# Kernel tuning notes

Hardware: AMD Instinct MI355X
Metric: run time of the kernel (lower is better)

## Reference

```python
import jax, jax.numpy as jnp
import numpy as np

FEATURE_DIM = 68
ONE_HOT_MAX = 29  # one-hot coordinate features only for coords < 29


def _compute_encodings(height, width):
    # height, width are static Python ints
    xs = jnp.arange(width, dtype=jnp.float32)
    ys = jnp.arange(height, dtype=jnp.float32)

    def axis_feats(coords, size):
        if size > 1:
            norm = 2.0 * (coords / (size - 1)) - 1.0
            angle = jnp.pi * (coords / (size - 1))
        else:
            norm = jnp.zeros_like(coords)
            angle = jnp.zeros_like(coords)
        sign = jnp.sign(coords - size / 2.0)  # -1 / 0 / +1 around midpoint
        rtan = jnp.round(jnp.tan(angle))
        return jnp.stack([norm, sign, jnp.sin(angle), jnp.cos(angle), rtan], axis=-1)  # [size, 5]

    xf = axis_feats(xs, width)    # [W, 5] -> feature slots 0,2,4,6,8
    yf = axis_feats(ys, height)   # [H, 5] -> feature slots 1,3,5,7,9

    xb = jnp.broadcast_to(xf[None, :, :], (height, width, 5))
    yb = jnp.broadcast_to(yf[:, None, :], (height, width, 5))
    # interleave x/y features -> order x0,y0,x1,y1,... matches slots 0..9
    first10 = jnp.stack([xb, yb], axis=-1).reshape(height, width, 10)

    idx = jnp.arange(ONE_HOT_MAX)
    ohx = (xs[:, None] == idx[None, :]).astype(jnp.float32)  # [W, 29], zero rows for x >= 29
    ohy = (ys[:, None] == idx[None, :]).astype(jnp.float32)  # [H, 29]
    ohx_b = jnp.broadcast_to(ohx[None, :, :], (height, width, ONE_HOT_MAX))
    ohy_b = jnp.broadcast_to(ohy[:, None, :], (height, width, ONE_HOT_MAX))

    return jnp.concatenate([first10, ohx_b, ohy_b], axis=-1)  # [H, W, 68]


def setup_inputs() -> dict:
    key = jax.random.key(0)
    H, W, B = 512, 512, 8
    x = jax.random.normal(key, (B, H * W), dtype=jnp.float32)
    return {"x": x, "height": H, "width": W}


def reference(x, height, width):
    batch_size, seq_len = x.shape
    enc = _compute_encodings(height, width).reshape(-1, FEATURE_DIM)  # [H*W, 68]
    enc_b = jnp.broadcast_to(enc[None, :, :], (batch_size, seq_len, FEATURE_DIM))
    return jnp.concatenate([x[..., None], enc_b], axis=-1)  # [B, H*W, 69]
```

## Files before the change

kernel.cpp:

```cpp
#include <hip/hip_runtime.h>
#include <math.h>

typedef float f32x4 __attribute__((ext_vector_type(4)));

#define NF 69u
#define TILE_ROWS 64u
#define BLOCK 256u

__global__ void pe_table_kernel(const int* __restrict__ hptr,
                                const int* __restrict__ wptr,
                                float* __restrict__ tab) {
    const int H = *hptr;
    const int W = *wptr;
    const int total = W + H;
    for (int i = (int)(blockIdx.x * blockDim.x + threadIdx.x); i < total;
         i += (int)(gridDim.x * blockDim.x)) {
        const bool is_y = (i >= W);
        const int c = is_y ? (i - W) : i;
        const int size = is_y ? H : W;
        double norm = 0.0, angle = 0.0;
        if (size > 1) {
            const double r = (double)c / (double)(size - 1);
            norm = 2.0 * r - 1.0;
            angle = M_PI * r;
        }
        const double d = (double)c - 0.5 * (double)size;
        const float sgn = (d > 0.0) ? 1.0f : ((d < 0.0) ? -1.0f : 0.0f);
        const int base = (is_y ? 5 * W : 0) + 5 * c;
        tab[base + 0] = (float)norm;
        tab[base + 1] = sgn;
        tab[base + 2] = (float)sin(angle);
        tab[base + 3] = (float)cos(angle);
        tab[base + 4] = (float)rint(tan(angle));
    }
}

__global__ __launch_bounds__(BLOCK) void pe_main_kernel(
    const float* __restrict__ x,
    const int* __restrict__ hptr, const int* __restrict__ wptr,
    const float* __restrict__ tab,
    float* __restrict__ out, unsigned int Q ) {
    __shared__ float lds[TILE_ROWS * NF];

    const unsigned int W = (unsigned int)*wptr;
    const unsigned int H = (unsigned int)*hptr;
    const unsigned int yoff = 5u * W;
    const unsigned int ntiles = (Q + TILE_ROWS - 1u) / TILE_ROWS;
    const unsigned int lane = threadIdx.x & 63u;
    const unsigned int wv = threadIdx.x >> 6;

    for (unsigned int T = blockIdx.x; T < ntiles; T += gridDim.x) {
        const unsigned int q = T * TILE_ROWS + lane;
        unsigned int w = 0u, h = 0u;
        float xv = 0.0f;
        const bool valid = q < Q;
        if (valid) {
            const unsigned int t = q / W;
            w = q - t * W;
            h = t - (t / H) * H;
            if (wv == 0u) xv = x[q];
        }

        for (unsigned int f = wv; f < NF; f += 4u) {
            float v;
            if (f == 0u) {
                v = xv;
            } else {
                const unsigned int g = f - 1u;
                if (g < 10u) {
                    const unsigned int feat = g >> 1;
                    v = (g & 1u) ? tab[yoff + 5u * h + feat]
                                 : tab[5u * w + feat];
                } else if (g < 39u) {
                    v = (w == g - 10u) ? 1.0f : 0.0f;
                } else {
                    v = (h == g - 39u) ? 1.0f : 0.0f;
                }
            }
            lds[lane * NF + f] = v;
        }
        __syncthreads();

        const unsigned int rows = (Q - T * TILE_ROWS < TILE_ROWS)
                                      ? (Q - T * TILE_ROWS) : TILE_ROWS;
        const unsigned int nfl = rows * NF;
        const unsigned int n4 = nfl >> 2;
        const size_t obase = (size_t)T * (size_t)(TILE_ROWS * NF);
        const f32x4* lp = (const f32x4*)lds;
        f32x4* op = (f32x4*)(out + obase);
        for (unsigned int j = threadIdx.x; j < n4; j += BLOCK)
            __builtin_nontemporal_store(lp[j], op + j);
        for (unsigned int j = (n4 << 2) + threadIdx.x; j < nfl; j += BLOCK)
            out[obase + j] = lds[j];
        __syncthreads();
    }
}

extern "C" void kernel_launch(void* const* d_in, const int* in_sizes, int n_in,
                              void* d_out, int out_size, void* d_ws, size_t ws_size,
                              hipStream_t stream) {
    const float* x = (const float*)d_in[0];
    const int* hptr = (const int*)d_in[1];
    const int* wptr = (const int*)d_in[2];
    float* out = (float*)d_out;
    float* tab = (float*)d_ws;

    pe_table_kernel<<<8, 256, 0, stream>>>(hptr, wptr, tab);

    const unsigned int Q = (unsigned int)in_sizes[0];
    const unsigned int ntiles = (Q + TILE_ROWS - 1u) / TILE_ROWS;
    unsigned int blocks = ntiles < 2048u ? ntiles : 2048u;
    if (blocks == 0u) blocks = 1u;
    pe_main_kernel<<<blocks, BLOCK, 0, stream>>>(x, hptr, wptr, tab, out, Q);
}
```

Before: 124.4 us.

## Double-buffer LDS tiles and overlap next-tile compute with global stores

```diff
diff --git a/kernel.cpp b/kernel.cpp
--- a/kernel.cpp
+++ b/kernel.cpp
@@ -5,6 +5,7 @@
 
 #define NF 69u
 #define TILE_ROWS 64u
+#define TILE_FLOATS (TILE_ROWS * NF)
 #define BLOCK 256u
 
 __global__ void pe_table_kernel(const int* __restrict__ hptr,
@@ -35,12 +36,46 @@
     }
 }
 
+__device__ __forceinline__ void pe_compute_tile(
+    float* __restrict__ buf, unsigned int T, unsigned int Q,
+    unsigned int W, unsigned int H, unsigned int yoff,
+    const float* __restrict__ x, const float* __restrict__ tab,
+    unsigned int lane, unsigned int wv) {
+    const unsigned int q = T * TILE_ROWS + lane;
+    unsigned int w = 0u, h = 0u;
+    float xv = 0.0f;
+    if (q < Q) {
+        const unsigned int t = q / W;
+        w = q - t * W;
+        h = t - (t / H) * H;
+        xv = x[q];
+    }
+    for (unsigned int f = wv; f < NF; f += 4u) {
+        float v;
+        if (f == 0u) {
+            v = xv;
+        } else {
+            const unsigned int g = f - 1u;
+            if (g < 10u) {
+                const unsigned int feat = g >> 1;
+                v = (g & 1u) ? tab[yoff + 5u * h + feat]
+                             : tab[5u * w + feat];
+            } else if (g < 39u) {
+                v = (w == g - 10u) ? 1.0f : 0.0f;
+            } else {
+                v = (h == g - 39u) ? 1.0f : 0.0f;
+            }
+        }
+        buf[lane * NF + f] = v;
+    }
+}
+
 __global__ __launch_bounds__(BLOCK) void pe_main_kernel(
     const float* __restrict__ x,
     const int* __restrict__ hptr, const int* __restrict__ wptr,
     const float* __restrict__ tab,
     float* __restrict__ out, unsigned int Q ) {
-    __shared__ float lds[TILE_ROWS * NF];
+    __shared__ float lds[2][TILE_FLOATS];
 
     const unsigned int W = (unsigned int)*wptr;
     const unsigned int H = (unsigned int)*hptr;
@@ -48,51 +83,33 @@
     const unsigned int ntiles = (Q + TILE_ROWS - 1u) / TILE_ROWS;
     const unsigned int lane = threadIdx.x & 63u;
     const unsigned int wv = threadIdx.x >> 6;
+    const unsigned int gstride = gridDim.x;
 
-    for (unsigned int T = blockIdx.x; T < ntiles; T += gridDim.x) {
-        const unsigned int q = T * TILE_ROWS + lane;
-        unsigned int w = 0u, h = 0u;
-        float xv = 0.0f;
-        const bool valid = q < Q;
-        if (valid) {
-            const unsigned int t = q / W;
-            w = q - t * W;
-            h = t - (t / H) * H;
-            if (wv == 0u) xv = x[q];
-        }
+    unsigned int T = blockIdx.x;
+    if (T >= ntiles) return;
 
-        for (unsigned int f = wv; f < NF; f += 4u) {
-            float v;
-            if (f == 0u) {
-                v = xv;
-            } else {
-                const unsigned int g = f - 1u;
-                if (g < 10u) {
-                    const unsigned int feat = g >> 1;
-                    v = (g & 1u) ? tab[yoff + 5u * h + feat]
-                                 : tab[5u * w + feat];
-                } else if (g < 39u) {
-                    v = (w == g - 10u) ? 1.0f : 0.0f;
-                } else {
-                    v = (h == g - 39u) ? 1.0f : 0.0f;
-                }
-            }
-            lds[lane * NF + f] = v;
-        }
-        __syncthreads();
+    pe_compute_tile(lds[0], T, Q, W, H, yoff, x, tab, lane, wv);
+    unsigned int cur = 0u;
 
-        const unsigned int rows = (Q - T * TILE_ROWS < TILE_ROWS)
-                                      ? (Q - T * TILE_ROWS) : TILE_ROWS;
+    for (; T < ntiles; T += gstride) {
+        asm volatile("s_waitcnt lgkmcnt(0)\n\ts_barrier" ::: "memory");
+
+        const unsigned int rem = Q - T * TILE_ROWS;
+        const unsigned int rows = rem < TILE_ROWS ? rem : TILE_ROWS;
         const unsigned int nfl = rows * NF;
         const unsigned int n4 = nfl >> 2;
-        const size_t obase = (size_t)T * (size_t)(TILE_ROWS * NF);
-        const f32x4* lp = (const f32x4*)lds;
+        const size_t obase = (size_t)T * (size_t)TILE_FLOATS;
+        const f32x4* lp = (const f32x4*)lds[cur];
         f32x4* op = (f32x4*)(out + obase);
         for (unsigned int j = threadIdx.x; j < n4; j += BLOCK)
             __builtin_nontemporal_store(lp[j], op + j);
         for (unsigned int j = (n4 << 2) + threadIdx.x; j < nfl; j += BLOCK)
-            out[obase + j] = lds[j];
-        __syncthreads();
+            __builtin_nontemporal_store(lds[cur][j], out + obase + j);
+
+        const unsigned int Tn = T + gstride;
+        if (Tn < ntiles)
+            pe_compute_tile(lds[cur ^ 1u], Tn, Q, W, H, yoff, x, tab, lane, wv);
+        cur ^= 1u;
     }
 }
 
```

After: 112.6 us. -9.5%, faster.

## Give each wave a private LDS tile and drop block-wide barriers

Applied to the files above, without the earlier changes.

```diff
diff --git a/kernel.cpp b/kernel.cpp
--- a/kernel.cpp
+++ b/kernel.cpp
@@ -4,8 +4,10 @@
 typedef float f32x4 __attribute__((ext_vector_type(4)));
 
 #define NF 69u
-#define TILE_ROWS 64u
+#define WROWS 64u
+#define WTILE_FLOATS (WROWS * NF)
 #define BLOCK 256u
+#define WAVES 4u
 
 __global__ void pe_table_kernel(const int* __restrict__ hptr,
                                 const int* __restrict__ wptr,
@@ -40,59 +42,62 @@
     const int* __restrict__ hptr, const int* __restrict__ wptr,
     const float* __restrict__ tab,
     float* __restrict__ out, unsigned int Q ) {
-    __shared__ float lds[TILE_ROWS * NF];
+    __shared__ __align__(16) float lds[WAVES][WTILE_FLOATS];
 
     const unsigned int W = (unsigned int)*wptr;
     const unsigned int H = (unsigned int)*hptr;
     const unsigned int yoff = 5u * W;
-    const unsigned int ntiles = (Q + TILE_ROWS - 1u) / TILE_ROWS;
     const unsigned int lane = threadIdx.x & 63u;
-    const unsigned int wv = threadIdx.x >> 6;
+    const unsigned int wid = threadIdx.x >> 6;
+    float* buf = lds[wid];
 
-    for (unsigned int T = blockIdx.x; T < ntiles; T += gridDim.x) {
-        const unsigned int q = T * TILE_ROWS + lane;
+    {
+        f32x4 z = {0.f, 0.f, 0.f, 0.f};
+        f32x4* bp = (f32x4*)buf;
+        for (unsigned int j = lane; j < WTILE_FLOATS / 4u; j += 64u)
+            bp[j] = z;
+    }
+
+    const unsigned int ntiles = (Q + WROWS - 1u) / WROWS;
+    const unsigned int gw = blockIdx.x * WAVES + wid;
+    const unsigned int nw = gridDim.x * WAVES;
+
+    for (unsigned int T = gw; T < ntiles; T += nw) {
+        const unsigned int q = T * WROWS + lane;
         unsigned int w = 0u, h = 0u;
-        float xv = 0.0f;
         const bool valid = q < Q;
         if (valid) {
             const unsigned int t = q / W;
             w = q - t * W;
             h = t - (t / H) * H;
-            if (wv == 0u) xv = x[q];
+            float* row = buf + lane * NF;
+            row[0] = x[q];
+#pragma unroll
+            for (unsigned int ft = 0u; ft < 5u; ++ft) {
+                row[1u + 2u * ft] = tab[5u * w + ft];
+                row[2u + 2u * ft] = tab[yoff + 5u * h + ft];
+            }
+            if (w < 29u) row[11u + w] = 1.0f;
+            if (h < 29u) row[40u + h] = 1.0f;
         }
 
-        for (unsigned int f = wv; f < NF; f += 4u) {
-            float v;
-            if (f == 0u) {
-                v = xv;
-            } else {
-                const unsigned int g = f - 1u;
-                if (g < 10u) {
-                    const unsigned int feat = g >> 1;
-                    v = (g & 1u) ? tab[yoff + 5u * h + feat]
-                                 : tab[5u * w + feat];
-                } else if (g < 39u) {
-                    v = (w == g - 10u) ? 1.0f : 0.0f;
-                } else {
-                    v = (h == g - 39u) ? 1.0f : 0.0f;
-                }
-            }
-            lds[lane * NF + f] = v;
-        }
-        __syncthreads();
-
-        const unsigned int rows = (Q - T * TILE_ROWS < TILE_ROWS)
-                                      ? (Q - T * TILE_ROWS) : TILE_ROWS;
+        const unsigned int rem = Q - T * WROWS;
+        const unsigned int rows = rem < WROWS ? rem : WROWS;
         const unsigned int nfl = rows * NF;
         const unsigned int n4 = nfl >> 2;
-        const size_t obase = (size_t)T * (size_t)(TILE_ROWS * NF);
-        const f32x4* lp = (const f32x4*)lds;
+        const size_t obase = (size_t)T * (size_t)WTILE_FLOATS;
+        const f32x4* lp = (const f32x4*)buf;
         f32x4* op = (f32x4*)(out + obase);
-        for (unsigned int j = threadIdx.x; j < n4; j += BLOCK)
+        for (unsigned int j = lane; j < n4; j += 64u)
             __builtin_nontemporal_store(lp[j], op + j);
-        for (unsigned int j = (n4 << 2) + threadIdx.x; j < nfl; j += BLOCK)
-            out[obase + j] = lds[j];
-        __syncthreads();
+        for (unsigned int j = (n4 << 2) + lane; j < nfl; j += 64u)
+            __builtin_nontemporal_store(buf[j], out + obase + j);
+
+        if (valid) {
+            float* row = buf + lane * NF;
+            if (w < 29u) row[11u + w] = 0.0f;
+            if (h < 29u) row[40u + h] = 0.0f;
+        }
     }
 }
 
@@ -108,8 +113,9 @@
     pe_table_kernel<<<8, 256, 0, stream>>>(hptr, wptr, tab);
 
     const unsigned int Q = (unsigned int)in_sizes[0];
-    const unsigned int ntiles = (Q + TILE_ROWS - 1u) / TILE_ROWS;
-    unsigned int blocks = ntiles < 2048u ? ntiles : 2048u;
+    const unsigned int ntiles = (Q + WROWS - 1u) / WROWS;
+    unsigned int blocks = (ntiles + WAVES - 1u) / WAVES;
+    if (blocks > 2048u) blocks = 2048u;
     if (blocks == 0u) blocks = 1u;
     pe_main_kernel<<<blocks, BLOCK, 0, stream>>>(x, hptr, wptr, tab, out, Q);
 }
```

After: 118.0 us. 5.2% less time.
